# Optimization experiments

Measured on AMD Instinct MI355X. Metric: run time of the kernel, lower is better.

## Reference

```python
import jax, jax.numpy as jnp
import numpy as np

B, S, E, H = 2, 2048, 1024, 16
D = E // H  # head dimension = 64


def setup_inputs() -> dict:
    key = jax.random.key(0)
    ks = jax.random.split(key, 12)
    scale_in = 1.0 / np.sqrt(E)
    x = jax.random.normal(ks[0], (B, S, E), dtype=jnp.float32)
    # random 0/1 attention mask (1 = attend, 0 = masked out)
    mask = jax.random.randint(ks[1], (B, S, S), 0, 2, dtype=jnp.int32)
    # per-head QKV projections, stacked over the head axis: [H, E, D]
    Wq = jax.random.normal(ks[2], (H, E, D), dtype=jnp.float32) * scale_in
    bq = jnp.zeros((H, D), dtype=jnp.float32)
    Wk = jax.random.normal(ks[3], (H, E, D), dtype=jnp.float32) * scale_in
    bk = jnp.zeros((H, D), dtype=jnp.float32)
    Wv = jax.random.normal(ks[4], (H, E, D), dtype=jnp.float32) * scale_in
    bv = jnp.zeros((H, D), dtype=jnp.float32)
    # output projection: [H*D, E] == [E, E]
    Wo = jax.random.normal(ks[5], (H * D, E), dtype=jnp.float32) * scale_in
    bo = jnp.zeros((E,), dtype=jnp.float32)
    return {"x": x, "mask": mask, "Wq": Wq, "bq": bq, "Wk": Wk, "bk": bk,
            "Wv": Wv, "bv": bv, "Wo": Wo, "bo": bo}


def reference(x, mask, Wq, bq, Wk, bk, Wv, bv, Wo, bo):
    # Batched equivalent of the per-head Python loop: all heads at once.
    q = jnp.einsum('bse,hed->bhsd', x, Wq) + bq[None, :, None, :]  # [B,H,S,D]
    k = jnp.einsum('bse,hed->bhsd', x, Wk) + bk[None, :, None, :]
    v = jnp.einsum('bse,hed->bhsd', x, Wv) + bv[None, :, None, :]
    scale = 1.0 / jnp.sqrt(jnp.asarray(D, dtype=q.dtype))
    scores = jnp.einsum('bhsd,bhtd->bhst', q, k) * scale          # [B,H,S,S]
    scores = jnp.where(mask[:, None, :, :] != 0, scores, jnp.asarray(-1e9, scores.dtype))
    attn = jax.nn.softmax(scores, axis=-1)
    ctx = jnp.einsum('bhst,bhtd->bhsd', attn, v)                  # [B,H,S,D]
    # concat heads along feature dim (torch.cat(dim=2))
    concat = jnp.transpose(ctx, (0, 2, 1, 3)).reshape(B, S, H * D)
    return concat @ Wo + bo
```

## Files before the change

### kernel.cpp

```cpp
#include <hip/hip_runtime.h>

#define S_LEN 2048
#define EMB   1024
#define NH    16
#define HD    64
#define BS    2
#define QSCALE 0.18033688f

typedef __bf16 bf16;
typedef bf16  bf16x8 __attribute__((ext_vector_type(8)));
typedef bf16  bf16x4 __attribute__((ext_vector_type(4)));
typedef float f32x4  __attribute__((ext_vector_type(4)));
typedef unsigned long long u64;
typedef unsigned int u32;

__device__ __forceinline__ bf16x8 ld8(const bf16* p){ return *(const bf16x8*)p; }

__device__ __forceinline__ void gl_lds16(const bf16* g, void* l) {
    __builtin_amdgcn_global_load_lds(
        (const __attribute__((address_space(1))) void*)g,
        (__attribute__((address_space(3))) void*)l,
        16, 0, 0);
}

#define SW(row, g) ((((g) ^ ((row) & 7))) * 8)

__global__ __launch_bounds__(256)
void pack_mask(const int* __restrict__ mask, u64* __restrict__ pm)
{
    int lane = threadIdx.x & 63;
    int row  = blockIdx.x * 4 + (threadIdx.x >> 6);
    const int* mr = mask + (size_t)row * S_LEN;
    u64* pr = pm + (size_t)row * (S_LEN / 64);
    for (int i = 0; i < S_LEN / 64; ++i) {
        u64 bits = __ballot(mr[i * 64 + lane] != 0);
        if (lane == 0) pr[i] = bits;
    }
}

__global__ __launch_bounds__(256)
void prep(const float* __restrict__ x, bf16* __restrict__ xbf,
          const int* __restrict__ mask, u64* __restrict__ pm,
          const float* __restrict__ W0, const float* __restrict__ W1,
          const float* __restrict__ W2, const float* __restrict__ W3,
          bf16* __restrict__ Wt)
{
    const int bid = blockIdx.x;
    const int tid = threadIdx.x;
    __shared__ float T[64][68];

    if (bid < 1024) {
        size_t i = ((size_t)bid * 256 + tid) * 16;
        bf16 t[16];
        #pragma unroll
        for (int g = 0; g < 4; ++g) {
            f32x4 v = *(const f32x4*)(x + i + g * 4);
            #pragma unroll
            for (int j = 0; j < 4; ++j) t[g * 4 + j] = (bf16)v[j];
        }
        *(bf16x8*)(xbf + i)     = *(bf16x8*)t;
        *(bf16x8*)(xbf + i + 8) = *(bf16x8*)(t + 8);
    } else if (bid < 2048) {
        int lane = tid & 63;
        int row  = (bid - 1024) * 4 + (tid >> 6);
        const int* mr = mask + (size_t)row * S_LEN;
        u64* pr = pm + (size_t)row * (S_LEN / 64);
        for (int i = 0; i < S_LEN / 64; ++i) {
            u64 bits = __ballot(mr[i * 64 + lane] != 0);
            if (lane == 0) pr[i] = bits;
        }
    } else {
        const int t   = bid - 2048;
        const int z   = t >> 8;
        const int rem = t & 255;
        const int k0 = (rem & 15) * 64, n0 = (rem >> 4) * 64;
        const float* W = z == 0 ? W0 : z == 1 ? W1 : z == 2 ? W2 : W3;
        const bool head = z < 3;
        {
            int k = k0 + (tid >> 2), cg = (tid & 3) * 16;
            size_t base = head ? ((size_t)(n0 >> 6) * ((size_t)EMB * HD) + (size_t)k * HD + cg)
                               : ((size_t)k * EMB + n0 + cg);
            #pragma unroll
            for (int g = 0; g < 4; ++g) {
                f32x4 v = *(const f32x4*)(W + base + g * 4);
                #pragma unroll
                for (int j = 0; j < 4; ++j) T[tid >> 2][cg + g * 4 + j] = v[j];
            }
        }
        __syncthreads();
        {
            int n = n0 + (tid >> 2), ck = (tid & 3) * 16;
            bf16 t16[16];
            #pragma unroll
            for (int j = 0; j < 16; ++j) t16[j] = (bf16)T[ck + j][tid >> 2];
            bf16* outp = Wt + (size_t)z * EMB * EMB + (size_t)n * EMB + k0 + ck;
            *(bf16x8*)outp       = *(bf16x8*)t16;
            *(bf16x8*)(outp + 8) = *(bf16x8*)(t16 + 8);
        }
    }
}

__global__ __launch_bounds__(256)
void scale_q(bf16* __restrict__ q)
{
    size_t i = ((size_t)blockIdx.x * 256 + threadIdx.x) * 8;
    bf16x8 v = *(bf16x8*)(q + i);
    #pragma unroll
    for (int j = 0; j < 8; ++j) v[j] = (bf16)((float)v[j] * QSCALE);
    *(bf16x8*)(q + i) = v;
}

__global__ __launch_bounds__(256, 3)
void gemm_qkv(const void* __restrict__ Ap, const bf16* __restrict__ Wt,
              const float* __restrict__ bqp, const float* __restrict__ bkp,
              const float* __restrict__ bvp,
              bf16* __restrict__ qb, bf16* __restrict__ kb, bf16* __restrict__ VT,
              int a32)
{
    const int tid  = threadIdx.x;
    const int lane = tid & 63, quad = lane >> 4, c = lane & 15;
    const int w = tid >> 6, wm = w >> 1, wn = w & 1;
    const int m0 = blockIdx.x * 128;
    const int n0 = blockIdx.y * 128;

    __shared__ bf16 Ash[128][64];
    __shared__ bf16 Wsh[128][64];
    __shared__ bf16 Ush[4][16][72];

    f32x4 acc[4][4];
    #pragma unroll
    for (int mt = 0; mt < 4; ++mt)
        #pragma unroll
        for (int nt = 0; nt < 4; ++nt) acc[mt][nt] = (f32x4){0.f,0.f,0.f,0.f};

    const int lrow = lane >> 3, lcol = (lane & 7) * 8;

    for (int k0 = 0; k0 < EMB; k0 += 64) {
        __syncthreads();
        if (!a32) {
            const bf16* A = (const bf16*)Ap;
            #pragma unroll
            for (int j = 0; j < 4; ++j)
                gl_lds16(A + (size_t)(m0 + w * 32 + j * 8 + lrow) * EMB + k0 + lcol,
                         &Ash[w * 32 + j * 8][0]);
        } else {
            const float* A = (const float*)Ap + (size_t)(m0 + (tid >> 1)) * EMB + k0 + (tid & 1) * 32;
            bf16 t[32];
            #pragma unroll
            for (int g = 0; g < 8; ++g) {
                f32x4 v = *(const f32x4*)(A + g * 4);
                #pragma unroll
                for (int j = 0; j < 4; ++j) t[g * 4 + j] = (bf16)v[j];
            }
            #pragma unroll
            for (int g2 = 0; g2 < 4; ++g2)
                *(bf16x8*)&Ash[tid >> 1][(tid & 1) * 32 + g2 * 8] = *(bf16x8*)(t + g2 * 8);
        }
        #pragma unroll
        for (int j = 0; j < 4; ++j)
            gl_lds16(Wt + (size_t)(n0 + w * 32 + j * 8 + lrow) * EMB + k0 + lcol,
                     &Wsh[w * 32 + j * 8][0]);
        __syncthreads();

        #pragma unroll
        for (int kh = 0; kh < 2; ++kh) {
            bf16x8 af[4], bfv[4];
            #pragma unroll
            for (int mt = 0; mt < 4; ++mt) af[mt]  = ld8(&Ash[wm * 64 + mt * 16 + c][kh * 32 + quad * 8]);
            #pragma unroll
            for (int nt = 0; nt < 4; ++nt) bfv[nt] = ld8(&Wsh[wn * 64 + nt * 16 + c][kh * 32 + quad * 8]);
            #pragma unroll
            for (int mt = 0; mt < 4; ++mt)
                #pragma unroll
                for (int nt = 0; nt < 4; ++nt)
                    acc[mt][nt] = __builtin_amdgcn_mfma_f32_16x16x32_bf16(af[mt], bfv[nt], acc[mt][nt], 0, 0, 0);
        }
    }

    const int z = n0 >> 10;
    const float* bias = z == 0 ? bqp : z == 1 ? bkp : bvp;
    if (z == 2) {
        #pragma unroll
        for (int nt = 0; nt < 4; ++nt) {
            int nn = (n0 & 1023) + wn * 64 + nt * 16 + c;
            float bv_ = bias[nn];
            int head = nn >> 6, d = nn & 63;
            #pragma unroll
            for (int mt = 0; mt < 4; ++mt) {
                int m = m0 + wm * 64 + mt * 16 + quad * 4;
                bf16x4 pv;
                #pragma unroll
                for (int r = 0; r < 4; ++r) pv[r] = (bf16)(acc[mt][nt][r] + bv_);
                *(bf16x4*)&VT[((size_t)((m >> 11) * NH + head) * HD + d) * S_LEN + (m & 2047)] = pv;
            }
        }
    } else {
        bf16* outb = z == 0 ? qb : kb;
        const float scl = z == 0 ? QSCALE : 1.0f;
        float bv4[4];
        #pragma unroll
        for (int nt = 0; nt < 4; ++nt) bv4[nt] = bias[(n0 & 1023) + wn * 64 + nt * 16 + c];
        #pragma unroll
        for (int mt = 0; mt < 4; ++mt) {
            #pragma unroll
            for (int nt = 0; nt < 4; ++nt)
                #pragma unroll
                for (int r = 0; r < 4; ++r)
                    Ush[w][quad * 4 + r][nt * 16 + c] = (bf16)((acc[mt][nt][r] + bv4[nt]) * scl);
            __builtin_amdgcn_s_waitcnt(0xc07f);
            int row16 = lane >> 2, cg = (lane & 3) * 16;
            int m = m0 + wm * 64 + mt * 16 + row16;
            int nn0 = (n0 & 1023) + wn * 64 + cg;
            bf16x8 v0 = *(bf16x8*)&Ush[w][row16][cg];
            bf16x8 v1 = *(bf16x8*)&Ush[w][row16][cg + 8];
            *(bf16x8*)&outb[(size_t)m * EMB + nn0]     = v0;
            *(bf16x8*)&outb[(size_t)m * EMB + nn0 + 8] = v1;
            __builtin_amdgcn_s_waitcnt(0xc07f);
        }
    }
}

__global__ __launch_bounds__(256, 3)
void gemm_o(const bf16* __restrict__ Ap, const bf16* __restrict__ Wt,
            const float* __restrict__ bo, float* __restrict__ C)
{
    const int tid  = threadIdx.x;
    const int lane = tid & 63, quad = lane >> 4, c = lane & 15;
    const int w = tid >> 6, wm = w >> 1, wn = w & 1;
    const int m0 = blockIdx.x * 128;
    const int n0 = blockIdx.y * 128;

    __shared__ bf16 Ash[128][64];
    __shared__ bf16 Wsh[128][64];

    f32x4 acc[4][4];
    #pragma unroll
    for (int mt = 0; mt < 4; ++mt)
        #pragma unroll
        for (int nt = 0; nt < 4; ++nt) acc[mt][nt] = (f32x4){0.f,0.f,0.f,0.f};

    const int lrow = lane >> 3, lcol = (lane & 7) * 8;

    for (int k0 = 0; k0 < EMB; k0 += 64) {
        __syncthreads();
        #pragma unroll
        for (int j = 0; j < 4; ++j)
            gl_lds16(Ap + (size_t)(m0 + w * 32 + j * 8 + lrow) * EMB + k0 + lcol,
                     &Ash[w * 32 + j * 8][0]);
        #pragma unroll
        for (int j = 0; j < 4; ++j)
            gl_lds16(Wt + (size_t)(n0 + w * 32 + j * 8 + lrow) * EMB + k0 + lcol,
                     &Wsh[w * 32 + j * 8][0]);
        __syncthreads();

        #pragma unroll
        for (int kh = 0; kh < 2; ++kh) {
            bf16x8 af[4], bfv[4];
            #pragma unroll
            for (int mt = 0; mt < 4; ++mt) af[mt]  = ld8(&Ash[wm * 64 + mt * 16 + c][kh * 32 + quad * 8]);
            #pragma unroll
            for (int nt = 0; nt < 4; ++nt) bfv[nt] = ld8(&Wsh[wn * 64 + nt * 16 + c][kh * 32 + quad * 8]);
            #pragma unroll
            for (int mt = 0; mt < 4; ++mt)
                #pragma unroll
                for (int nt = 0; nt < 4; ++nt)
                    acc[mt][nt] = __builtin_amdgcn_mfma_f32_16x16x32_bf16(af[mt], bfv[nt], acc[mt][nt], 0, 0, 0);
        }
    }

    #pragma unroll
    for (int nt = 0; nt < 4; ++nt) {
        int n = n0 + wn * 64 + nt * 16 + c;
        float bv_ = bo[n];
        #pragma unroll
        for (int mt = 0; mt < 4; ++mt)
            #pragma unroll
            for (int r = 0; r < 4; ++r) {
                int m = m0 + wm * 64 + mt * 16 + quad * 4 + r;
                C[(size_t)m * EMB + n] = acc[mt][nt][r] + bv_;
            }
    }
}

__global__ __launch_bounds__(512)
void gemm128(const void* __restrict__ Ap, const float* __restrict__ Wp,
             const bf16* __restrict__ Wtp, const float* __restrict__ bias,
             void* __restrict__ Cp, int N, int K, int whead,
             int m_base, int a32, int cmode)
{
    const int tid  = threadIdx.x;
    const int lane = tid & 63, quad = lane >> 4, c = lane & 15;
    const int w = tid >> 6, wm = w >> 2, wn = w & 3;
    const int m0 = blockIdx.x * 128, n0 = blockIdx.y * 128;

    __shared__ bf16 Ash[128][64];
    __shared__ bf16 Wsh[128][64];

    f32x4 acc[4][2];
    #pragma unroll
    for (int mt = 0; mt < 4; ++mt)
        #pragma unroll
        for (int nt = 0; nt < 2; ++nt) acc[mt][nt] = (f32x4){0.f,0.f,0.f,0.f};

    const int arow = tid >> 2, aq = tid & 3;

    auto compute = [&]() {
        #pragma unroll
        for (int kh = 0; kh < 2; ++kh) {
            bf16x8 bfr[2];
            #pragma unroll
            for (int nt = 0; nt < 2; ++nt) {
                int rw = wn * 32 + nt * 16 + c;
                bfr[nt] = ld8(&Wsh[rw][SW(rw, kh * 4 + quad)]);
            }
            #pragma unroll
            for (int mt = 0; mt < 4; ++mt) {
                int ra = wm * 64 + mt * 16 + c;
                bf16x8 af = ld8(&Ash[ra][SW(ra, kh * 4 + quad)]);
                #pragma unroll
                for (int nt = 0; nt < 2; ++nt)
                    acc[mt][nt] = __builtin_amdgcn_mfma_f32_16x16x32_bf16(af, bfr[nt], acc[mt][nt], 0, 0, 0);
            }
        }
    };

    for (int k0 = 0; k0 < K; k0 += 64) {
        __syncthreads();
        if (a32) {
            const float* A = (const float*)Ap + (size_t)(m_base + m0 + arow) * K + k0 + aq * 16;
            bf16 t16[16];
            #pragma unroll
            for (int g = 0; g < 4; ++g) {
                f32x4 v = *(const f32x4*)(A + g * 4);
                #pragma unroll
                for (int j = 0; j < 4; ++j) t16[g * 4 + j] = (bf16)v[j];
            }
            *(bf16x8*)&Ash[arow][SW(arow, aq * 2)]     = *(bf16x8*)t16;
            *(bf16x8*)&Ash[arow][SW(arow, aq * 2 + 1)] = *(bf16x8*)(t16 + 8);
        } else {
            const bf16* A = (const bf16*)Ap + (size_t)(m_base + m0 + arow) * K + k0 + aq * 16;
            *(bf16x8*)&Ash[arow][SW(arow, aq * 2)]     = ld8(A);
            *(bf16x8*)&Ash[arow][SW(arow, aq * 2 + 1)] = ld8(A + 8);
        }
        {
            int nl = tid & 127, kg = tid >> 7;
            int n = n0 + nl;
            size_t base    = whead ? ((size_t)(n >> 6) * ((size_t)K * HD) + (n & 63))
                                   : (size_t)n;
            size_t kstride = whead ? (size_t)HD : (size_t)N;
            #pragma unroll
            for (int p = 0; p < 2; ++p) {
                int grp = kg + 4 * p;
                bf16 t8[8];
                #pragma unroll
                for (int j = 0; j < 8; ++j)
                    t8[j] = (bf16)Wp[base + (size_t)(k0 + grp * 8 + j) * kstride];
                *(bf16x8*)&Wsh[nl][SW(nl, grp)] = *(bf16x8*)t8;
            }
        }
        __syncthreads();
        compute();
    }

    #pragma unroll
    for (int nt = 0; nt < 2; ++nt) {
        int n = n0 + wn * 32 + nt * 16 + c;
        float bv_ = bias[n];
        #pragma unroll
        for (int mt = 0; mt < 4; ++mt)
            #pragma unroll
            for (int r = 0; r < 4; ++r) {
                int m = m0 + wm * 64 + mt * 16 + quad * 4 + r;
                float v = acc[mt][nt][r] + bv_;
                if (cmode == 0)      ((bf16*)Cp)[(size_t)m * N + n] = (bf16)v;
                else if (cmode == 1) ((float*)Cp)[(size_t)m * N + n] = v;
                else {
                    int mm = m_base + m;
                    ((bf16*)Cp)[((size_t)((mm >> 11) * NH + (n >> 6)) * HD + (n & 63)) * S_LEN + (mm & 2047)] = (bf16)v;
                }
            }
    }
}

__global__ __launch_bounds__(512, 2)
void attn_kernel(bf16* q0p, bf16* q1p, const bf16* __restrict__ kbuf,
                 const bf16* __restrict__ VTg, const u64* __restrict__ pmask)
{
    const int tid  = threadIdx.x;
    const int w    = tid >> 6;
    const int lane = tid & 63;
    const int quad = lane >> 4;
    const int c    = lane & 15;
    const int flat  = blockIdx.y * 16 + blockIdx.x;
    const int flat2 = (flat & 7) * 64 + (flat >> 3);
    const int q0   = (flat2 & 15) * 128;
    const int bh   = flat2 >> 4;
    const int b    = bh >> 4, h = bh & 15;

    bf16* qc = b ? q1p : q0p;
    const bf16* kh_ = kbuf + (size_t)b * S_LEN * EMB + h * HD;
    const bf16* vt  = VTg + (size_t)bh * HD * S_LEN;

    __shared__ bf16 Ksh [2][64][64];
    __shared__ bf16 VTsh[2][64][64];
    __shared__ bf16 Psh[8][16][64];

    bf16x8 qf[2];
    #pragma unroll
    for (int kk = 0; kk < 2; ++kk)
        qf[kk] = ld8(qc + (size_t)(q0 + w * 16 + c) * EMB + h * HD + kk * 32 + quad * 8);

    const u64* pmr = pmask + (size_t)(b * S_LEN + q0 + w * 16 + c) * (S_LEN / 64);

    f32x4 l4 = (f32x4){0.f,0.f,0.f,0.f};
    f32x4 o[4];
    #pragma unroll
    for (int dt = 0; dt < 4; ++dt) o[dt] = (f32x4){0.f,0.f,0.f,0.f};

    const int srow = tid >> 3, sg = tid & 7;
    bf16x8 kr, vr;
    auto loadKV = [&](int t0) {
        kr = ld8(kh_ + (size_t)(t0 + srow) * EMB + sg * 8);
        vr = ld8(vt + (size_t)srow * S_LEN + t0 + sg * 8);
    };

    loadKV(0);
    int buf = 0;
    for (int t0 = 0; t0 < S_LEN; t0 += 64) {
        *(bf16x8*)&Ksh [buf][srow][SW(srow, sg)] = kr;
        *(bf16x8*)&VTsh[buf][srow][SW(srow, sg)] = vr;
        __syncthreads();
        if (t0 + 64 < S_LEN) loadKV(t0 + 64);

        u64 s0 = pmr[t0 >> 6] >> (quad * 4);
        u32 mm[2] = {(u32)s0, (u32)(s0 >> 32)};

        f32x4 sc[4];
        #pragma unroll
        for (int tt = 0; tt < 4; ++tt) sc[tt] = (f32x4){0.f,0.f,0.f,0.f};
        #pragma unroll
        for (int tt = 0; tt < 4; ++tt)
            #pragma unroll
            for (int kk = 0; kk < 2; ++kk) {
                int rk = tt * 16 + c;
                bf16x8 ka = ld8(&Ksh[buf][rk][SW(rk, kk * 4 + quad)]);
                sc[tt] = __builtin_amdgcn_mfma_f32_16x16x32_bf16(ka, qf[kk], sc[tt], 0, 0, 0);
            }

        #pragma unroll
        for (int tt = 0; tt < 4; ++tt) {
            u32 half = mm[tt >> 1];
            bf16x4 pv;
            #pragma unroll
            for (int r = 0; r < 4; ++r) {
                float e = __builtin_amdgcn_exp2f(sc[tt][r]);
                e = ((half >> ((tt & 1) * 16 + r)) & 1) ? e : 0.f;
                l4[r] += e;
                pv[r] = (bf16)e;
            }
            *(bf16x4*)&Psh[w][c][SW(c, tt * 2 + (quad >> 1)) + (quad & 1) * 4] = pv;
        }
        __builtin_amdgcn_s_waitcnt(0xc07f);

        #pragma unroll
        for (int th = 0; th < 2; ++th) {
            bf16x8 pf = ld8(&Psh[w][c][SW(c, th * 4 + quad)]);
            #pragma unroll
            for (int dt = 0; dt < 4; ++dt) {
                int rv = dt * 16 + c;
                bf16x8 av = ld8(&VTsh[buf][rv][SW(rv, th * 4 + quad)]);
                o[dt] = __builtin_amdgcn_mfma_f32_16x16x32_bf16(av, pf, o[dt], 0, 0, 0);
            }
        }
        buf ^= 1;
    }

    float ls = l4[0] + l4[1] + l4[2] + l4[3];
    ls += __shfl_xor(ls, 16);
    ls += __shfl_xor(ls, 32);
    float inv = 1.0f / fmaxf(ls, 1e-30f);
    #pragma unroll
    for (int dt = 0; dt < 4; ++dt) {
        bf16x4 ov;
        #pragma unroll
        for (int r = 0; r < 4; ++r) ov[r] = (bf16)(o[dt][r] * inv);
        *(bf16x4*)&qc[(size_t)(q0 + w * 16 + c) * EMB + h * HD + dt * 16 + quad * 4] = ov;
    }
}

extern "C" void kernel_launch(void* const* d_in, const int* in_sizes, int n_in,
                              void* d_out, int out_size, void* d_ws, size_t ws_size,
                              hipStream_t stream)
{
    const float* x    = (const float*)d_in[0];
    const int*   mask = (const int*)d_in[1];
    const float* Wq   = (const float*)d_in[2];
    const float* bq   = (const float*)d_in[3];
    const float* Wk   = (const float*)d_in[4];
    const float* bk   = (const float*)d_in[5];
    const float* Wv   = (const float*)d_in[6];
    const float* bv   = (const float*)d_in[7];
    const float* Wo   = (const float*)d_in[8];
    const float* bo   = (const float*)d_in[9];
    float* out = (float*)d_out;

    const size_t SLAB = (size_t)S_LEN * EMB;
    const size_t QB = (size_t)BS * SLAB * sizeof(bf16);
    const size_t WT = (size_t)4 * EMB * EMB * sizeof(bf16);
    const size_t PM = (size_t)BS * S_LEN * (S_LEN / 64) * 8;
    const size_t XB = (size_t)BS * SLAB * sizeof(bf16);

    bf16* VT = (bf16*)d_out;
    bf16* kb = (bf16*)d_out + BS * SLAB;

    dim3 b256(256), b512(512);
    dim3 gAtt (S_LEN / 128, BS * NH);
    dim3 gPk  (BS * S_LEN / 4);
    dim3 gFull(BS * S_LEN / 128, EMB / 128);
    dim3 gHalf(S_LEN / 128, EMB / 128);

    if (ws_size >= QB + WT + PM + XB + 64) {
        bf16* qb  = (bf16*)d_ws;
        bf16* Wt  = (bf16*)((char*)d_ws + QB);
        u64*  pm  = (u64*)((char*)d_ws + QB + WT);
        bf16* xbf = (bf16*)((char*)d_ws + QB + WT + PM);

        prep<<<dim3(3072), b256, 0, stream>>>(x, xbf, mask, pm, Wq, Wk, Wv, Wo, Wt);

        gemm_qkv<<<dim3(BS * S_LEN / 128, 3 * EMB / 128), b256, 0, stream>>>(
            xbf, Wt, bq, bk, bv, qb, kb, VT, 0);

        attn_kernel<<<gAtt, b512, 0, stream>>>(qb, qb + SLAB, kb, VT, pm);

        gemm_o<<<dim3(BS * S_LEN / 128, EMB / 128), b256, 0, stream>>>(
            qb, Wt + (size_t)3 * EMB * EMB, bo, out);
    } else if (ws_size >= QB + PM + 64) {
        bf16* qb = (bf16*)d_ws;
        u64*  pm = (u64*)((char*)d_ws + QB);
        pack_mask<<<gPk, b256, 0, stream>>>(mask, pm);

        gemm128<<<gFull, b512, 0, stream>>>(x, Wk, nullptr, bk, kb, EMB, EMB, 1, 0, 1, 0);
        gemm128<<<gFull, b512, 0, stream>>>(x, Wv, nullptr, bv, VT, EMB, EMB, 1, 0, 1, 2);
        gemm128<<<gFull, b512, 0, stream>>>(x, Wq, nullptr, bq, qb, EMB, EMB, 1, 0, 1, 0);
        scale_q<<<dim3(BS * SLAB / (256 * 8)), b256, 0, stream>>>(qb);

        attn_kernel<<<gAtt, b512, 0, stream>>>(qb, qb + SLAB, kb, VT, pm);

        gemm128<<<gFull, b512, 0, stream>>>(qb, Wo, nullptr, bo, out, EMB, EMB, 0, 0, 0, 1);
    } else {
        bf16* qb0 = (bf16*)d_in[4];
        bf16* qb1 = (bf16*)d_in[6];
        u64*  pm  = (u64*)d_in[2];

        gemm128<<<gFull, b512, 0, stream>>>(x, Wk, nullptr, bk, kb, EMB, EMB, 1, 0, 1, 0);
        gemm128<<<gFull, b512, 0, stream>>>(x, Wv, nullptr, bv, VT, EMB, EMB, 1, 0, 1, 2);
        gemm128<<<gHalf, b512, 0, stream>>>(x, Wq, nullptr, bq, qb0, EMB, EMB, 1, 0,     1, 0);
        gemm128<<<gHalf, b512, 0, stream>>>(x, Wq, nullptr, bq, qb1, EMB, EMB, 1, S_LEN, 1, 0);
        scale_q<<<dim3(SLAB / (256 * 8)), b256, 0, stream>>>(qb0);
        scale_q<<<dim3(SLAB / (256 * 8)), b256, 0, stream>>>(qb1);
        pack_mask<<<gPk, b256, 0, stream>>>(mask, pm);

        attn_kernel<<<gAtt, b512, 0, stream>>>(qb0, qb1, kb, VT, pm);

        gemm128<<<gHalf, b512, 0, stream>>>(qb0, Wo, nullptr, bo, out,        EMB, EMB, 0, 0, 0, 1);
        gemm128<<<gHalf, b512, 0, stream>>>(qb1, Wo, nullptr, bo, out + SLAB, EMB, EMB, 0, 0, 0, 1);
    }
}
```

Baseline: 235.7 us.

## Remap GEMM blocks per XCD, halve gemm_o N-tile, stage output stores via LDS

Both projection GEMMs now remap the flat block index so that each of the 8 XCDs works on a contiguous rectangle of M/N tiles, which should improve L2 reuse of A and W. gemm_o uses a 128x64 tile instead of 128x128, doubling the grid to 512 blocks for better CU fill, and raises the launch-bounds occupancy hint from 3 to 4. Its epilogue now stages fp32 results through LDS so the global writes are coalesced 16-byte vector stores rather than scattered scalar ones. The cost is more blocks re-reading A tiles and hardcoded grid-shape assumptions in the swizzle.

```diff
diff --git a/kernel.cpp b/kernel.cpp
--- a/kernel.cpp
+++ b/kernel.cpp
@@ -120,8 +120,10 @@
     const int tid  = threadIdx.x;
     const int lane = tid & 63, quad = lane >> 4, c = lane & 15;
     const int w = tid >> 6, wm = w >> 1, wn = w & 1;
-    const int m0 = blockIdx.x * 128;
-    const int n0 = blockIdx.y * 128;
+    const int flat = blockIdx.y * 32 + blockIdx.x;
+    const int xcd = flat & 7, li = flat >> 3;
+    const int m0 = ((xcd >> 1) * 8 + (li & 7)) * 128;
+    const int n0 = ((xcd & 1) * 12 + (li >> 3)) * 128;
 
     __shared__ bf16 Ash[128][64];
     __shared__ bf16 Wsh[128][64];
@@ -220,24 +222,26 @@
     }
 }
 
-__global__ __launch_bounds__(256, 3)
+__global__ __launch_bounds__(256, 4)
 void gemm_o(const bf16* __restrict__ Ap, const bf16* __restrict__ Wt,
             const float* __restrict__ bo, float* __restrict__ C)
 {
     const int tid  = threadIdx.x;
     const int lane = tid & 63, quad = lane >> 4, c = lane & 15;
     const int w = tid >> 6, wm = w >> 1, wn = w & 1;
-    const int m0 = blockIdx.x * 128;
-    const int n0 = blockIdx.y * 128;
+    const int flat = blockIdx.y * 32 + blockIdx.x;
+    const int xcd = flat & 7, li = flat >> 3;
+    const int m0 = ((xcd >> 1) * 8 + (li & 7)) * 128;
+    const int n0 = ((xcd & 1) * 8 + (li >> 3)) * 64;
 
     __shared__ bf16 Ash[128][64];
-    __shared__ bf16 Wsh[128][64];
-
-    f32x4 acc[4][4];
+    __shared__ bf16 Wsh[64][64];
+
+    f32x4 acc[4][2];
     #pragma unroll
     for (int mt = 0; mt < 4; ++mt)
         #pragma unroll
-        for (int nt = 0; nt < 4; ++nt) acc[mt][nt] = (f32x4){0.f,0.f,0.f,0.f};
+        for (int nt = 0; nt < 2; ++nt) acc[mt][nt] = (f32x4){0.f,0.f,0.f,0.f};
 
     const int lrow = lane >> 3, lcol = (lane & 7) * 8;
 
@@ -248,37 +252,47 @@
             gl_lds16(Ap + (size_t)(m0 + w * 32 + j * 8 + lrow) * EMB + k0 + lcol,
                      &Ash[w * 32 + j * 8][0]);
         #pragma unroll
-        for (int j = 0; j < 4; ++j)
-            gl_lds16(Wt + (size_t)(n0 + w * 32 + j * 8 + lrow) * EMB + k0 + lcol,
-                     &Wsh[w * 32 + j * 8][0]);
+        for (int j = 0; j < 2; ++j)
+            gl_lds16(Wt + (size_t)(n0 + w * 16 + j * 8 + lrow) * EMB + k0 + lcol,
+                     &Wsh[w * 16 + j * 8][0]);
         __syncthreads();
 
         #pragma unroll
         for (int kh = 0; kh < 2; ++kh) {
-            bf16x8 af[4], bfv[4];
+            bf16x8 af[4], bfv[2];
             #pragma unroll
             for (int mt = 0; mt < 4; ++mt) af[mt]  = ld8(&Ash[wm * 64 + mt * 16 + c][kh * 32 + quad * 8]);
             #pragma unroll
-            for (int nt = 0; nt < 4; ++nt) bfv[nt] = ld8(&Wsh[wn * 64 + nt * 16 + c][kh * 32 + quad * 8]);
+            for (int nt = 0; nt < 2; ++nt) bfv[nt] = ld8(&Wsh[wn * 32 + nt * 16 + c][kh * 32 + quad * 8]);
             #pragma unroll
             for (int mt = 0; mt < 4; ++mt)
                 #pragma unroll
-                for (int nt = 0; nt < 4; ++nt)
+                for (int nt = 0; nt < 2; ++nt)
                     acc[mt][nt] = __builtin_amdgcn_mfma_f32_16x16x32_bf16(af[mt], bfv[nt], acc[mt][nt], 0, 0, 0);
         }
     }
 
-    #pragma unroll
-    for (int nt = 0; nt < 4; ++nt) {
-        int n = n0 + wn * 64 + nt * 16 + c;
-        float bv_ = bo[n];
-        #pragma unroll
-        for (int mt = 0; mt < 4; ++mt)
-            #pragma unroll
-            for (int r = 0; r < 4; ++r) {
-                int m = m0 + wm * 64 + mt * 16 + quad * 4 + r;
-                C[(size_t)m * EMB + n] = acc[mt][nt][r] + bv_;
-            }
+    __syncthreads();
+    float (*Ush)[16][36] = (float(*)[16][36])&Ash[0][0];
+    float bv2[2];
+    #pragma unroll
+    for (int nt = 0; nt < 2; ++nt) bv2[nt] = bo[n0 + wn * 32 + nt * 16 + c];
+    #pragma unroll
+    for (int mt = 0; mt < 4; ++mt) {
+        #pragma unroll
+        for (int nt = 0; nt < 2; ++nt)
+            #pragma unroll
+            for (int r = 0; r < 4; ++r)
+                Ush[w][quad * 4 + r][nt * 16 + c] = acc[mt][nt][r] + bv2[nt];
+        __builtin_amdgcn_s_waitcnt(0xc07f);
+        int row16 = lane >> 2, cg = (lane & 3) * 8;
+        int m = m0 + wm * 64 + mt * 16 + row16;
+        int nn = n0 + wn * 32 + cg;
+        f32x4 v0 = *(f32x4*)&Ush[w][row16][cg];
+        f32x4 v1 = *(f32x4*)&Ush[w][row16][cg + 4];
+        *(f32x4*)&C[(size_t)m * EMB + nn]     = v0;
+        *(f32x4*)&C[(size_t)m * EMB + nn + 4] = v1;
+        __builtin_amdgcn_s_waitcnt(0xc07f);
     }
 }
 
@@ -532,7 +546,7 @@
 
         attn_kernel<<<gAtt, b512, 0, stream>>>(qb, qb + SLAB, kb, VT, pm);
 
-        gemm_o<<<dim3(BS * S_LEN / 128, EMB / 128), b256, 0, stream>>>(
+        gemm_o<<<dim3(BS * S_LEN / 128, EMB / 64), b256, 0, stream>>>(
             qb, Wt + (size_t)3 * EMB * EMB, bo, out);
     } else if (ws_size >= QB + PM + 64) {
         bf16* qb = (bf16*)d_ws;
```

Result: no change. 232.3 us, median of 2 (-1.4%).
